# Optimization experiments

Hardware: AMD Instinct MI355X
Metric: run time of the kernel (lower is better)

Reference implementation:

```python
import jax, jax.numpy as jnp
import numpy as np

E = 16          # n_routed_experts
D = 2048        # embedding_dim
H = 1408        # moe_inter_dim
HS = 2 * 1408   # shared expert hidden (n_shared_experts * moe_inter_dim)
TOP_K = 6
ROUTE_SCALE = 1.0


def setup_inputs() -> dict:
    key = jax.random.key(0)
    ks = jax.random.split(key, 16)
    s = 0.02
    return {
        "x": jax.random.normal(ks[0], (4, 1024, D), dtype=jnp.float32),
        "gate_w": jax.random.normal(ks[1], (E, D), dtype=jnp.float32) * s,
        "gate_b": jax.random.normal(ks[2], (E,), dtype=jnp.float32) * s,
        "w1": jax.random.normal(ks[3], (E, H, D), dtype=jnp.float32) * s,
        "b1": jax.random.normal(ks[4], (E, H), dtype=jnp.float32) * s,
        "w2": jax.random.normal(ks[5], (E, D, H), dtype=jnp.float32) * s,
        "b2": jax.random.normal(ks[6], (E, D), dtype=jnp.float32) * s,
        "w3": jax.random.normal(ks[7], (E, H, D), dtype=jnp.float32) * s,
        "b3": jax.random.normal(ks[8], (E, H), dtype=jnp.float32) * s,
        "ws1": jax.random.normal(ks[9], (HS, D), dtype=jnp.float32) * s,
        "bs1": jax.random.normal(ks[10], (HS,), dtype=jnp.float32) * s,
        "ws2": jax.random.normal(ks[11], (D, HS), dtype=jnp.float32) * s,
        "bs2": jax.random.normal(ks[12], (D,), dtype=jnp.float32) * s,
        "ws3": jax.random.normal(ks[13], (HS, D), dtype=jnp.float32) * s,
        "bs3": jax.random.normal(ks[14], (HS,), dtype=jnp.float32) * s,
    }


def reference(x, gate_w, gate_b, w1, b1, w2, b2, w3, b3, ws1, bs1, ws2, bs2, ws3, bs3):
    shape = x.shape
    xf = x.reshape(-1, shape[-1])                       # [T, D]
    # --- Gate ---
    scores = xf @ gate_w.T                              # [T, E]
    probs = jax.nn.softmax(scores.astype(jnp.float32), axis=-1)
    biased = probs + gate_b                             # bias added after softmax
    _, idx = jax.lax.top_k(biased, TOP_K)               # [T, K]
    weights = jnp.take_along_axis(probs, idx, axis=1) * ROUTE_SCALE
    weights = weights.astype(x.dtype)                   # [T, K]
    # Combine weights as dense [T, E] (sum of top-k routing weights per expert)
    onehot = jax.nn.one_hot(idx, E, dtype=weights.dtype)  # [T, K, E]
    cw = jnp.einsum('tk,tke->te', weights, onehot)        # [T, E]
    # --- Routed experts: scan over experts, accumulate weighted SwiGLU outputs ---
    def expert_step(y, params):
        W1, B1, W2, B2, W3, B3, c = params              # c: [T]
        h = jax.nn.silu(xf @ W1.T + B1) * (xf @ W3.T + B3)  # [T, H]
        out = h @ W2.T + B2                             # [T, D]
        return y + c[:, None] * out, None
    y0 = jnp.zeros_like(xf)
    y, _ = jax.lax.scan(expert_step, y0, (w1, b1, w2, b2, w3, b3, cw.T))
    # --- Shared experts (dense SwiGLU MLP) ---
    z = (jax.nn.silu(xf @ ws1.T + bs1) * (xf @ ws3.T + bs3)) @ ws2.T + bs2
    return (y + z).reshape(shape)
```

## Files before the change

### kernel.cpp

```cpp
#include <hip/hip_runtime.h>

#define NE 16
#define DD 2048
#define HH 1408
#define HSH 2816
#define TOPK 6
#define TT 4096

typedef __bf16 bf16x8 __attribute__((ext_vector_type(8)));
typedef __bf16 bf16x4 __attribute__((ext_vector_type(4)));
typedef float f32x4 __attribute__((ext_vector_type(4)));

typedef const __attribute__((address_space(1))) void gvoid_t;
typedef __attribute__((address_space(3))) void lvoid_t;

__device__ __forceinline__ void gll16(const void* g, void* l) {
  __builtin_amdgcn_global_load_lds((gvoid_t*)g, (lvoid_t*)l, 16, 0, 0);
}

__global__ void k_cvt(const float* __restrict__ s, __bf16* __restrict__ d, long n4) {
  long i = (long)blockIdx.x * blockDim.x + threadIdx.x;
  long stride = (long)gridDim.x * blockDim.x;
  for (; i < n4; i += stride) {
    float4 v = ((const float4*)s)[i];
    bf16x4 o = { (__bf16)v.x, (__bf16)v.y, (__bf16)v.z, (__bf16)v.w };
    ((bf16x4*)d)[i] = o;
  }
}

__global__ __launch_bounds__(256) void k_gate(
    const float* __restrict__ x, const float* __restrict__ gw,
    const float* __restrict__ gb, float* __restrict__ cw,
    int* __restrict__ counts, int* __restrict__ lists) {
  int t = blockIdx.x;
  int lane = threadIdx.x & 63, wave = threadIdx.x >> 6;
  __shared__ float sc[NE];
  const float* xt = x + (size_t)t * DD;
  for (int ei = 0; ei < 4; ++ei) {
    int e = wave * 4 + ei;
    const float* ge = gw + (size_t)e * DD;
    float s = 0.f;
    for (int j = 0; j < DD / 64; ++j) s += xt[lane + 64 * j] * ge[lane + 64 * j];
    for (int o = 32; o; o >>= 1) s += __shfl_xor(s, o);
    if (lane == 0) sc[e] = s;
  }
  __syncthreads();
  if (threadIdx.x == 0) {
    float p[NE], b[NE];
    float m = -1e30f;
    for (int e = 0; e < NE; ++e) m = fmaxf(m, sc[e]);
    float sum = 0.f;
    for (int e = 0; e < NE; ++e) { p[e] = expf(sc[e] - m); sum += p[e]; }
    float inv = 1.f / sum;
    for (int e = 0; e < NE; ++e) { p[e] *= inv; b[e] = p[e] + gb[e]; }
    float out[NE];
    bool used[NE];
    for (int e = 0; e < NE; ++e) { out[e] = 0.f; used[e] = false; }
    for (int k = 0; k < TOPK; ++k) {
      int best = -1; float bv = -1e30f;
      for (int e = 0; e < NE; ++e)
        if (!used[e] && b[e] > bv) { bv = b[e]; best = e; }
      used[best] = true;
      out[best] = p[best];
      int pos = atomicAdd(&counts[best], 1);
      lists[best * TT + pos] = t;
    }
    for (int e = 0; e < NE; ++e) cw[(size_t)t * NE + e] = out[e];
  }
}

__global__ void k_offsets(const int* __restrict__ counts, int* __restrict__ offs) {
  if (threadIdx.x == 0) {
    int a = 0;
    for (int e = 0; e < NE; ++e) { offs[e] = a; a += counts[e]; }
    offs[NE] = a;
  }
}

template <bool GATHER>
__global__ __launch_bounds__(256, 2) void k_gemm1(
    const __bf16* __restrict__ xb,
    const __bf16* __restrict__ W1, const float* __restrict__ B1,
    const __bf16* __restrict__ W3, const float* __restrict__ B3,
    __bf16* __restrict__ Hout, int Hdim,
    const int* __restrict__ counts, const int* __restrict__ offs,
    const int* __restrict__ lists) {
  int e = blockIdx.z;
  int count = GATHER ? counts[e] : TT;
  int m0 = blockIdx.y * 128;
  if (m0 >= count) return;
  int n0 = blockIdx.x * 64;
  const __bf16* W1e = W1 + (size_t)e * Hdim * DD;
  const __bf16* W3e = W3 + (size_t)e * Hdim * DD;
  const float* B1e = B1 + (size_t)e * Hdim;
  const float* B3e = B3 + (size_t)e * Hdim;
  int hbase = GATHER ? offs[e] : 0;
  const int* liste = GATHER ? lists + (size_t)e * TT : nullptr;

  __shared__ __bf16 At[128 * 64];
  __shared__ __bf16 B1t[64 * 64];
  __shared__ __bf16 B3t[64 * 64];
  __shared__ int rowtok[128];

  int tid = threadIdx.x, lane = tid & 63, wave = tid >> 6;
  if (tid < 128) {
    int s = m0 + tid;
    rowtok[tid] = GATHER ? liste[s < count ? s : 0] : (m0 + tid);
  }
  __syncthreads();

  int wm = wave >> 1, wn = wave & 1;
  f32x4 acc1[4][2] = {};
  f32x4 acc3[4][2] = {};
  int lr8 = lane >> 3;
  int lc8 = (lane & 7) * 8;
  int fr = lane & 15;
  int fk = (lane >> 4) * 8;

  for (int k0 = 0; k0 < DD; k0 += 64) {
    #pragma unroll
    for (int c = 0; c < 4; ++c) {
      int br = c * 32 + wave * 8;
      int tok = rowtok[br + lr8];
      gll16(xb + (size_t)tok * DD + k0 + lc8, &At[br * 64]);
    }
    #pragma unroll
    for (int c = 0; c < 2; ++c) {
      int br = c * 32 + wave * 8;
      gll16(W1e + (size_t)(n0 + br + lr8) * DD + k0 + lc8, &B1t[br * 64]);
      gll16(W3e + (size_t)(n0 + br + lr8) * DD + k0 + lc8, &B3t[br * 64]);
    }
    __syncthreads();
    #pragma unroll
    for (int kk = 0; kk < 2; ++kk) {
      bf16x8 af[4], b1f[2], b3f[2];
      #pragma unroll
      for (int m = 0; m < 4; ++m)
        af[m] = *(const bf16x8*)&At[(wm * 64 + m * 16 + fr) * 64 + kk * 32 + fk];
      #pragma unroll
      for (int n = 0; n < 2; ++n) {
        b1f[n] = *(const bf16x8*)&B1t[(wn * 32 + n * 16 + fr) * 64 + kk * 32 + fk];
        b3f[n] = *(const bf16x8*)&B3t[(wn * 32 + n * 16 + fr) * 64 + kk * 32 + fk];
      }
      #pragma unroll
      for (int m = 0; m < 4; ++m)
        #pragma unroll
        for (int n = 0; n < 2; ++n) {
          acc1[m][n] = __builtin_amdgcn_mfma_f32_16x16x32_bf16(af[m], b1f[n], acc1[m][n], 0, 0, 0);
          acc3[m][n] = __builtin_amdgcn_mfma_f32_16x16x32_bf16(af[m], b3f[n], acc3[m][n], 0, 0, 0);
        }
    }
    __syncthreads();
  }
  #pragma unroll
  for (int m = 0; m < 4; ++m)
    #pragma unroll
    for (int n = 0; n < 2; ++n)
      #pragma unroll
      for (int j = 0; j < 4; ++j) {
        int rl = wm * 64 + m * 16 + (lane >> 4) * 4 + j;
        int s = m0 + rl;
        if (s < count) {
          int col = n0 + wn * 32 + n * 16 + fr;
          float h1 = acc1[m][n][j] + B1e[col];
          float h3 = acc3[m][n][j] + B3e[col];
          float v = h1 / (1.f + expf(-h1)) * h3;
          Hout[(size_t)(hbase + s) * Hdim + col] = (__bf16)v;
        }
      }
}

template <bool GATHER>
__global__ __launch_bounds__(256, 2) void k_gemm2(
    const __bf16* __restrict__ Hsrc, int Kd,
    const __bf16* __restrict__ W2, const float* __restrict__ B2,
    float* __restrict__ out, const float* __restrict__ cw,
    const int* __restrict__ counts, const int* __restrict__ offs,
    const int* __restrict__ lists) {
  int e = blockIdx.z;
  int count = GATHER ? counts[e] : TT;
  int m0 = blockIdx.y * 128;
  if (m0 >= count) return;
  int n0 = blockIdx.x * 64;
  const __bf16* Ae = Hsrc + (size_t)(GATHER ? offs[e] : 0) * Kd;
  const __bf16* W2e = W2 + (size_t)e * DD * Kd;
  const float* B2e = B2 + (size_t)(GATHER ? e * DD : 0);
  const int* liste = GATHER ? lists + (size_t)e * TT : nullptr;

  __shared__ __bf16 At[128 * 64];
  __shared__ __bf16 Bt[64 * 64];
  __shared__ int rowtok[128];

  int tid = threadIdx.x, lane = tid & 63, wave = tid >> 6;
  if (GATHER && tid < 128) {
    int s = m0 + tid;
    rowtok[tid] = liste[s < count ? s : 0];
  }
  __syncthreads();

  int wm = wave >> 1, wn = wave & 1;
  f32x4 acc[4][2] = {};
  int lr8 = lane >> 3;
  int lc8 = (lane & 7) * 8;
  int fr = lane & 15;
  int fk = (lane >> 4) * 8;

  for (int k0 = 0; k0 < Kd; k0 += 64) {
    #pragma unroll
    for (int c = 0; c < 4; ++c) {
      int br = c * 32 + wave * 8;
      int sr = m0 + br + lr8;
      if (sr >= count) sr = count - 1;
      gll16(Ae + (size_t)sr * Kd + k0 + lc8, &At[br * 64]);
    }
    #pragma unroll
    for (int c = 0; c < 2; ++c) {
      int br = c * 32 + wave * 8;
      gll16(W2e + (size_t)(n0 + br + lr8) * Kd + k0 + lc8, &Bt[br * 64]);
    }
    __syncthreads();
    #pragma unroll
    for (int kk = 0; kk < 2; ++kk) {
      bf16x8 af[4], bf[2];
      #pragma unroll
      for (int m = 0; m < 4; ++m)
        af[m] = *(const bf16x8*)&At[(wm * 64 + m * 16 + fr) * 64 + kk * 32 + fk];
      #pragma unroll
      for (int n = 0; n < 2; ++n)
        bf[n] = *(const bf16x8*)&Bt[(wn * 32 + n * 16 + fr) * 64 + kk * 32 + fk];
      #pragma unroll
      for (int m = 0; m < 4; ++m)
        #pragma unroll
        for (int n = 0; n < 2; ++n)
          acc[m][n] = __builtin_amdgcn_mfma_f32_16x16x32_bf16(af[m], bf[n], acc[m][n], 0, 0, 0);
    }
    __syncthreads();
  }
  #pragma unroll
  for (int m = 0; m < 4; ++m)
    #pragma unroll
    for (int n = 0; n < 2; ++n)
      #pragma unroll
      for (int j = 0; j < 4; ++j) {
        int rl = wm * 64 + m * 16 + (lane >> 4) * 4 + j;
        int s = m0 + rl;
        if (s < count) {
          int d = n0 + wn * 32 + n * 16 + fr;
          float v = acc[m][n][j] + B2e[d];
          if (GATHER) {
            int tok = rowtok[rl];
            v *= cw[(size_t)tok * NE + e];
            atomicAdd(&out[(size_t)tok * DD + d], v);
          } else {
            atomicAdd(&out[(size_t)s * DD + d], v);
          }
        }
      }
}

extern "C" void kernel_launch(void* const* d_in, const int* in_sizes, int n_in,
                              void* d_out, int out_size, void* d_ws, size_t ws_size,
                              hipStream_t stream) {
  const float* x      = (const float*)d_in[0];
  const float* gate_w = (const float*)d_in[1];
  const float* gate_b = (const float*)d_in[2];
  const float* w1     = (const float*)d_in[3];
  const float* b1     = (const float*)d_in[4];
  const float* w2     = (const float*)d_in[5];
  const float* b2     = (const float*)d_in[6];
  const float* w3     = (const float*)d_in[7];
  const float* b3     = (const float*)d_in[8];
  const float* ws1    = (const float*)d_in[9];
  const float* bs1    = (const float*)d_in[10];
  const float* ws2    = (const float*)d_in[11];
  const float* bs2    = (const float*)d_in[12];
  const float* ws3    = (const float*)d_in[13];
  const float* bs3    = (const float*)d_in[14];
  float* outp = (float*)d_out;

  char* ws = (char*)d_ws;
  size_t off = 0;
  auto take = [&](size_t bytes) { char* p = ws + off; off += (bytes + 255) & ~(size_t)255; return p; };
  __bf16* xb   = (__bf16*)take((size_t)TT * DD * 2);
  __bf16* w1b  = (__bf16*)take((size_t)NE * HH * DD * 2);
  __bf16* w3b  = (__bf16*)take((size_t)NE * HH * DD * 2);
  __bf16* w2b  = (__bf16*)take((size_t)NE * DD * HH * 2);
  __bf16* ws1b = (__bf16*)take((size_t)HSH * DD * 2);
  __bf16* ws3b = (__bf16*)take((size_t)HSH * DD * 2);
  __bf16* ws2b = (__bf16*)take((size_t)DD * HSH * 2);
  __bf16* Hbuf = (__bf16*)take((size_t)TT * TOPK * HH * 2);
  __bf16* Sbuf = (__bf16*)take((size_t)TT * HSH * 2);
  float*  cw   = (float*)take((size_t)TT * NE * 4);
  int*    lists  = (int*)take((size_t)NE * TT * 4);
  int*    counts = (int*)take(64);
  int*    offs   = (int*)take(128);

  hipMemsetAsync(d_out, 0, (size_t)TT * DD * sizeof(float), stream);
  hipMemsetAsync(counts, 0, NE * sizeof(int), stream);

  k_cvt<<<2048, 256, 0, stream>>>(x, xb, (long)TT * DD / 4);
  k_cvt<<<2048, 256, 0, stream>>>(w1, w1b, (long)NE * HH * DD / 4);
  k_cvt<<<2048, 256, 0, stream>>>(w3, w3b, (long)NE * HH * DD / 4);
  k_cvt<<<2048, 256, 0, stream>>>(w2, w2b, (long)NE * DD * HH / 4);
  k_cvt<<<2048, 256, 0, stream>>>(ws1, ws1b, (long)HSH * DD / 4);
  k_cvt<<<2048, 256, 0, stream>>>(ws3, ws3b, (long)HSH * DD / 4);
  k_cvt<<<2048, 256, 0, stream>>>(ws2, ws2b, (long)DD * HSH / 4);

  k_gate<<<TT, 256, 0, stream>>>(x, gate_w, gate_b, cw, counts, lists);
  k_offsets<<<1, 64, 0, stream>>>(counts, offs);

  k_gemm1<true><<<dim3(HH / 64, TT / 128, NE), 256, 0, stream>>>(
      xb, w1b, b1, w3b, b3, Hbuf, HH, counts, offs, lists);
  k_gemm1<false><<<dim3(HSH / 64, TT / 128, 1), 256, 0, stream>>>(
      xb, ws1b, bs1, ws3b, bs3, Sbuf, HSH, nullptr, nullptr, nullptr);
  k_gemm2<true><<<dim3(DD / 64, TT / 128, NE), 256, 0, stream>>>(
      Hbuf, HH, w2b, b2, outp, cw, counts, offs, lists);
  k_gemm2<false><<<dim3(DD / 64, TT / 128, 1), 256, 0, stream>>>(
      Sbuf, HSH, ws2b, bs2, outp, nullptr, nullptr, nullptr, nullptr);
}
```

Measured before the change: 1.470 ms.

## Widen GEMM N-tiles to 128 and replace atomic scatter with gather-based combine

Both expert GEMM kernels now use 128-wide N tiles with a 4x4 accumulator per wave, which doubles the reuse of each loaded A tile and halves the number of blocks. The routed second GEMM no longer does weighted float atomicAdds into the output. It writes per-assignment bf16 results into a scratch buffer that reuses the w1b region, and a new combine kernel gathers each token's six rows using the token-to-position maps recorded by the gate. The shared-expert GEMM2 writes the output directly, so the output memset is gone. The cost is higher register pressure from the larger accumulators, an extra kernel pass, and bf16 rounding of expert outputs before they are combined.

After: 1.519 ms. 3.3% more time.

```diff
diff --git a/kernel.cpp b/kernel.cpp
--- a/kernel.cpp
+++ b/kernel.cpp
@@ -31,7 +31,8 @@
 __global__ __launch_bounds__(256) void k_gate(
     const float* __restrict__ x, const float* __restrict__ gw,
     const float* __restrict__ gb, float* __restrict__ cw,
-    int* __restrict__ counts, int* __restrict__ lists) {
+    int* __restrict__ counts, int* __restrict__ lists,
+    int* __restrict__ tok_e, int* __restrict__ tok_pos) {
   int t = blockIdx.x;
   int lane = threadIdx.x & 63, wave = threadIdx.x >> 6;
   __shared__ float sc[NE];
@@ -64,6 +65,8 @@
       out[best] = p[best];
       int pos = atomicAdd(&counts[best], 1);
       lists[best * TT + pos] = t;
+      tok_e[t * TOPK + k] = best;
+      tok_pos[t * TOPK + k] = pos;
     }
     for (int e = 0; e < NE; ++e) cw[(size_t)t * NE + e] = out[e];
   }
@@ -89,7 +92,7 @@
   int count = GATHER ? counts[e] : TT;
   int m0 = blockIdx.y * 128;
   if (m0 >= count) return;
-  int n0 = blockIdx.x * 64;
+  int n0 = blockIdx.x * 128;
   const __bf16* W1e = W1 + (size_t)e * Hdim * DD;
   const __bf16* W3e = W3 + (size_t)e * Hdim * DD;
   const float* B1e = B1 + (size_t)e * Hdim;
@@ -98,8 +101,8 @@
   const int* liste = GATHER ? lists + (size_t)e * TT : nullptr;
 
   __shared__ __bf16 At[128 * 64];
-  __shared__ __bf16 B1t[64 * 64];
-  __shared__ __bf16 B3t[64 * 64];
+  __shared__ __bf16 B1t[128 * 64];
+  __shared__ __bf16 B3t[128 * 64];
   __shared__ int rowtok[128];
 
   int tid = threadIdx.x, lane = tid & 63, wave = tid >> 6;
@@ -110,8 +113,8 @@
   __syncthreads();
 
   int wm = wave >> 1, wn = wave & 1;
-  f32x4 acc1[4][2] = {};
-  f32x4 acc3[4][2] = {};
+  f32x4 acc1[4][4] = {};
+  f32x4 acc3[4][4] = {};
   int lr8 = lane >> 3;
   int lc8 = (lane & 7) * 8;
   int fr = lane & 15;
@@ -123,29 +126,25 @@
       int br = c * 32 + wave * 8;
       int tok = rowtok[br + lr8];
       gll16(xb + (size_t)tok * DD + k0 + lc8, &At[br * 64]);
-    }
-    #pragma unroll
-    for (int c = 0; c < 2; ++c) {
-      int br = c * 32 + wave * 8;
       gll16(W1e + (size_t)(n0 + br + lr8) * DD + k0 + lc8, &B1t[br * 64]);
       gll16(W3e + (size_t)(n0 + br + lr8) * DD + k0 + lc8, &B3t[br * 64]);
     }
     __syncthreads();
     #pragma unroll
     for (int kk = 0; kk < 2; ++kk) {
-      bf16x8 af[4], b1f[2], b3f[2];
+      bf16x8 af[4], b1f[4], b3f[4];
       #pragma unroll
       for (int m = 0; m < 4; ++m)
         af[m] = *(const bf16x8*)&At[(wm * 64 + m * 16 + fr) * 64 + kk * 32 + fk];
       #pragma unroll
-      for (int n = 0; n < 2; ++n) {
-        b1f[n] = *(const bf16x8*)&B1t[(wn * 32 + n * 16 + fr) * 64 + kk * 32 + fk];
-        b3f[n] = *(const bf16x8*)&B3t[(wn * 32 + n * 16 + fr) * 64 + kk * 32 + fk];
+      for (int n = 0; n < 4; ++n) {
+        b1f[n] = *(const bf16x8*)&B1t[(wn * 64 + n * 16 + fr) * 64 + kk * 32 + fk];
+        b3f[n] = *(const bf16x8*)&B3t[(wn * 64 + n * 16 + fr) * 64 + kk * 32 + fk];
       }
       #pragma unroll
       for (int m = 0; m < 4; ++m)
         #pragma unroll
-        for (int n = 0; n < 2; ++n) {
+        for (int n = 0; n < 4; ++n) {
           acc1[m][n] = __builtin_amdgcn_mfma_f32_16x16x32_bf16(af[m], b1f[n], acc1[m][n], 0, 0, 0);
           acc3[m][n] = __builtin_amdgcn_mfma_f32_16x16x32_bf16(af[m], b3f[n], acc3[m][n], 0, 0, 0);
         }
@@ -155,13 +154,13 @@
   #pragma unroll
   for (int m = 0; m < 4; ++m)
     #pragma unroll
-    for (int n = 0; n < 2; ++n)
+    for (int n = 0; n < 4; ++n)
       #pragma unroll
       for (int j = 0; j < 4; ++j) {
         int rl = wm * 64 + m * 16 + (lane >> 4) * 4 + j;
         int s = m0 + rl;
         if (s < count) {
-          int col = n0 + wn * 32 + n * 16 + fr;
+          int col = n0 + wn * 64 + n * 16 + fr;
           float h1 = acc1[m][n][j] + B1e[col];
           float h3 = acc3[m][n][j] + B3e[col];
           float v = h1 / (1.f + expf(-h1)) * h3;
@@ -174,32 +173,24 @@
 __global__ __launch_bounds__(256, 2) void k_gemm2(
     const __bf16* __restrict__ Hsrc, int Kd,
     const __bf16* __restrict__ W2, const float* __restrict__ B2,
-    float* __restrict__ out, const float* __restrict__ cw,
-    const int* __restrict__ counts, const int* __restrict__ offs,
-    const int* __restrict__ lists) {
+    float* __restrict__ out, __bf16* __restrict__ Ybuf,
+    const int* __restrict__ counts, const int* __restrict__ offs) {
   int e = blockIdx.z;
   int count = GATHER ? counts[e] : TT;
   int m0 = blockIdx.y * 128;
   if (m0 >= count) return;
-  int n0 = blockIdx.x * 64;
-  const __bf16* Ae = Hsrc + (size_t)(GATHER ? offs[e] : 0) * Kd;
+  int n0 = blockIdx.x * 128;
+  int hbase = GATHER ? offs[e] : 0;
+  const __bf16* Ae = Hsrc + (size_t)hbase * Kd;
   const __bf16* W2e = W2 + (size_t)e * DD * Kd;
   const float* B2e = B2 + (size_t)(GATHER ? e * DD : 0);
-  const int* liste = GATHER ? lists + (size_t)e * TT : nullptr;
 
   __shared__ __bf16 At[128 * 64];
-  __shared__ __bf16 Bt[64 * 64];
-  __shared__ int rowtok[128];
+  __shared__ __bf16 Bt[128 * 64];
 
   int tid = threadIdx.x, lane = tid & 63, wave = tid >> 6;
-  if (GATHER && tid < 128) {
-    int s = m0 + tid;
-    rowtok[tid] = liste[s < count ? s : 0];
-  }
-  __syncthreads();
-
   int wm = wave >> 1, wn = wave & 1;
-  f32x4 acc[4][2] = {};
+  f32x4 acc[4][4] = {};
   int lr8 = lane >> 3;
   int lc8 = (lane & 7) * 8;
   int fr = lane & 15;
@@ -212,26 +203,22 @@
       int sr = m0 + br + lr8;
       if (sr >= count) sr = count - 1;
       gll16(Ae + (size_t)sr * Kd + k0 + lc8, &At[br * 64]);
-    }
-    #pragma unroll
-    for (int c = 0; c < 2; ++c) {
-      int br = c * 32 + wave * 8;
       gll16(W2e + (size_t)(n0 + br + lr8) * Kd + k0 + lc8, &Bt[br * 64]);
     }
     __syncthreads();
     #pragma unroll
     for (int kk = 0; kk < 2; ++kk) {
-      bf16x8 af[4], bf[2];
+      bf16x8 af[4], bf[4];
       #pragma unroll
       for (int m = 0; m < 4; ++m)
         af[m] = *(const bf16x8*)&At[(wm * 64 + m * 16 + fr) * 64 + kk * 32 + fk];
       #pragma unroll
-      for (int n = 0; n < 2; ++n)
-        bf[n] = *(const bf16x8*)&Bt[(wn * 32 + n * 16 + fr) * 64 + kk * 32 + fk];
+      for (int n = 0; n < 4; ++n)
+        bf[n] = *(const bf16x8*)&Bt[(wn * 64 + n * 16 + fr) * 64 + kk * 32 + fk];
       #pragma unroll
       for (int m = 0; m < 4; ++m)
         #pragma unroll
-        for (int n = 0; n < 2; ++n)
+        for (int n = 0; n < 4; ++n)
           acc[m][n] = __builtin_amdgcn_mfma_f32_16x16x32_bf16(af[m], bf[n], acc[m][n], 0, 0, 0);
     }
     __syncthreads();
@@ -239,23 +226,53 @@
   #pragma unroll
   for (int m = 0; m < 4; ++m)
     #pragma unroll
-    for (int n = 0; n < 2; ++n)
+    for (int n = 0; n < 4; ++n)
       #pragma unroll
       for (int j = 0; j < 4; ++j) {
         int rl = wm * 64 + m * 16 + (lane >> 4) * 4 + j;
         int s = m0 + rl;
         if (s < count) {
-          int d = n0 + wn * 32 + n * 16 + fr;
+          int d = n0 + wn * 64 + n * 16 + fr;
           float v = acc[m][n][j] + B2e[d];
-          if (GATHER) {
-            int tok = rowtok[rl];
-            v *= cw[(size_t)tok * NE + e];
-            atomicAdd(&out[(size_t)tok * DD + d], v);
-          } else {
-            atomicAdd(&out[(size_t)s * DD + d], v);
-          }
+          if (GATHER)
+            Ybuf[(size_t)(hbase + s) * DD + d] = (__bf16)v;
+          else
+            out[(size_t)s * DD + d] = v;
         }
       }
+}
+
+__global__ __launch_bounds__(256) void k_combine(
+    const __bf16* __restrict__ Ybuf, const float* __restrict__ cw,
+    const int* __restrict__ offs, const int* __restrict__ tok_e,
+    const int* __restrict__ tok_pos, float* __restrict__ out) {
+  int t = blockIdx.x;
+  int tid = threadIdx.x;
+  __shared__ int rws[TOPK];
+  __shared__ float wsh[TOPK];
+  if (tid < TOPK) {
+    int e = tok_e[t * TOPK + tid];
+    rws[tid] = offs[e] + tok_pos[t * TOPK + tid];
+    wsh[tid] = cw[(size_t)t * NE + e];
+  }
+  __syncthreads();
+  int d0 = tid * 8;
+  float a[8];
+  float4 o0 = *(const float4*)&out[(size_t)t * DD + d0];
+  float4 o1 = *(const float4*)&out[(size_t)t * DD + d0 + 4];
+  a[0] = o0.x; a[1] = o0.y; a[2] = o0.z; a[3] = o0.w;
+  a[4] = o1.x; a[5] = o1.y; a[6] = o1.z; a[7] = o1.w;
+  #pragma unroll
+  for (int k = 0; k < TOPK; ++k) {
+    bf16x8 v = *(const bf16x8*)&Ybuf[(size_t)rws[k] * DD + d0];
+    float w = wsh[k];
+    #pragma unroll
+    for (int j = 0; j < 8; ++j) a[j] += w * (float)v[j];
+  }
+  float4 r0 = { a[0], a[1], a[2], a[3] };
+  float4 r1 = { a[4], a[5], a[6], a[7] };
+  *(float4*)&out[(size_t)t * DD + d0] = r0;
+  *(float4*)&out[(size_t)t * DD + d0 + 4] = r1;
 }
 
 extern "C" void kernel_launch(void* const* d_in, const int* in_sizes, int n_in,
@@ -292,10 +309,12 @@
   __bf16* Sbuf = (__bf16*)take((size_t)TT * HSH * 2);
   float*  cw   = (float*)take((size_t)TT * NE * 4);
   int*    lists  = (int*)take((size_t)NE * TT * 4);
+  int*    tok_e  = (int*)take((size_t)TT * TOPK * 4);
+  int*    tok_pos= (int*)take((size_t)TT * TOPK * 4);
   int*    counts = (int*)take(64);
   int*    offs   = (int*)take(128);
-
-  hipMemsetAsync(d_out, 0, (size_t)TT * DD * sizeof(float), stream);
+  __bf16* Ybuf = w1b;
+
   hipMemsetAsync(counts, 0, NE * sizeof(int), stream);
 
   k_cvt<<<2048, 256, 0, stream>>>(x, xb, (long)TT * DD / 4);
@@ -306,15 +325,16 @@
   k_cvt<<<2048, 256, 0, stream>>>(ws3, ws3b, (long)HSH * DD / 4);
   k_cvt<<<2048, 256, 0, stream>>>(ws2, ws2b, (long)DD * HSH / 4);
 
-  k_gate<<<TT, 256, 0, stream>>>(x, gate_w, gate_b, cw, counts, lists);
+  k_gate<<<TT, 256, 0, stream>>>(x, gate_w, gate_b, cw, counts, lists, tok_e, tok_pos);
   k_offsets<<<1, 64, 0, stream>>>(counts, offs);
 
-  k_gemm1<true><<<dim3(HH / 64, TT / 128, NE), 256, 0, stream>>>(
+  k_gemm1<true><<<dim3(HH / 128, TT / 128, NE), 256, 0, stream>>>(
       xb, w1b, b1, w3b, b3, Hbuf, HH, counts, offs, lists);
-  k_gemm1<false><<<dim3(HSH / 64, TT / 128, 1), 256, 0, stream>>>(
+  k_gemm1<false><<<dim3(HSH / 128, TT / 128, 1), 256, 0, stream>>>(
       xb, ws1b, bs1, ws3b, bs3, Sbuf, HSH, nullptr, nullptr, nullptr);
-  k_gemm2<true><<<dim3(DD / 64, TT / 128, NE), 256, 0, stream>>>(
-      Hbuf, HH, w2b, b2, outp, cw, counts, offs, lists);
-  k_gemm2<false><<<dim3(DD / 64, TT / 128, 1), 256, 0, stream>>>(
-      Sbuf, HSH, ws2b, bs2, outp, nullptr, nullptr, nullptr, nullptr);
-}
+  k_gemm2<true><<<dim3(DD / 128, TT / 128, NE), 256, 0, stream>>>(
+      Hbuf, HH, w2b, b2, nullptr, Ybuf, counts, offs);
+  k_gemm2<false><<<dim3(DD / 128, TT / 128, 1), 256, 0, stream>>>(
+      Sbuf, HSH, ws2b, bs2, outp, nullptr, nullptr, nullptr);
+  k_combine<<<TT, 256, 0, stream>>>(Ybuf, cw, offs, tok_e, tok_pos, outp);
+}
```
